# Optimization experiments

Measured on AMD Instinct MI355X. Metric: run time of the kernel, lower is better.

The kernel has to match this reference:

```python
import jax, jax.numpy as jnp
import numpy as np

TOPK = 2
ALPHA = 32.0
EPS = 1e-20


def setup_inputs() -> dict:
    key = jax.random.key(0)
    ks = jax.random.split(key, 6)
    E, D, R, Q, V = 16, 2048, 16, 2048, 512
    B, S = 2, 2048
    return {
        "hidden_states": jax.random.normal(ks[0], (B, S, D), jnp.float32),
        "router_weight": jax.random.normal(ks[1], (E, D), jnp.float32) * 0.02,
        "q_lora_a": jax.random.normal(ks[2], (E, D, R), jnp.float32) * 0.02,
        "q_lora_b": jax.random.normal(ks[3], (E, R, Q), jnp.float32) * 0.02,
        "v_lora_a": jax.random.normal(ks[4], (E, D, R), jnp.float32) * 0.02,
        "v_lora_b": jax.random.normal(ks[5], (E, R, V), jnp.float32) * 0.02,
    }


def reference(hidden_states, router_weight, q_lora_a, q_lora_b, v_lora_a, v_lora_b):
    E, D, R = q_lora_a.shape
    Qo = q_lora_b.shape[-1]
    Vo = v_lora_b.shape[-1]
    scale = ALPHA / float(R)
    orig_shape = hidden_states.shape[:-1]
    h = hidden_states.reshape(-1, D)  # [n, D]
    n = h.shape[0]

    # router: top-k softmax probs, renormalized over the k selected experts
    logits = jnp.einsum('nd,ed->ne', h, router_weight)
    probs = jax.nn.softmax(logits, axis=-1)
    scores, idx = jax.lax.top_k(probs, TOPK)          # [n, k]
    scores = scores / (scores.sum(-1, keepdims=True) + EPS)

    # per-token expert combine weights c[n, e] = scale * sum_k score_k * 1[idx_k == e]
    c = jnp.zeros((n, E), h.dtype).at[jnp.arange(n)[:, None], idx].add(scores * scale)

    # dense per-expert low-rank projections; weighting by c makes non-selected
    # experts contribute zero -> identical math to gather + einsum + weighted sum.
    q_low = jnp.einsum('nd,edr->ner', h, q_lora_a) * c[..., None]  # [n, E, R]
    v_low = jnp.einsum('nd,edr->ner', h, v_lora_a) * c[..., None]
    q_delta = jnp.einsum('ner,erq->nq', q_low, q_lora_b)
    v_delta = jnp.einsum('ner,erv->nv', v_low, v_lora_b)

    return (q_delta.reshape(*orig_shape, Qo), v_delta.reshape(*orig_shape, Vo))
```

## Files before the change

kernel.cpp:

```cpp
#include <hip/hip_runtime.h>
#include <math.h>

#define DD 2048
#define EE 16
#define RR 16
#define QO 2048
#define VO 512
#define DSPLIT 4
#define DRANGE (DD / DSPLIT)
#define DC 64
#define ASTR 20
#define RDC 256
#define DSPL 8
#define TW 4
#define TBI (TW * 4)
#define ABLK 16
#define T2 32
#define CGQ (QO / 256)
#define CGV (VO / 256)

struct Route { int i0, i1; float w0, w1; };

__global__ __launch_bounds__(256) void logits_kernel(
    const float* __restrict__ h, const float* __restrict__ rw,
    double* __restrict__ lgp, int* __restrict__ cnt, int n)
{
    __shared__ float hs[8 * RDC];

    if (blockIdx.x == 0 && blockIdx.y == 0 && threadIdx.x < EE)
        cnt[threadIdx.x] = 0;

    int t0 = blockIdx.x * 8;
    int ds = blockIdx.y;
    int d0 = ds * RDC;
    int e  = threadIdx.x >> 4;
    int l  = threadIdx.x & 15;

    for (int i = threadIdx.x; i < 8 * (RDC / 4); i += 256) {
        int t = i >> 6, dq = (i & 63) * 4;
        float4 v = make_float4(0.f, 0.f, 0.f, 0.f);
        if (t0 + t < n)
            v = *(const float4*)&h[(size_t)(t0 + t) * DD + d0 + dq];
        *(float4*)&hs[t * RDC + dq] = v;
    }
    __syncthreads();

    double acc[8];
#pragma unroll
    for (int t = 0; t < 8; ++t) acc[t] = 0.0;

    const float* rwe = rw + e * DD + d0;
#pragma unroll
    for (int g = 0; g < RDC / 64; ++g) {
        int d = g * 64 + l * 4;
        float4 r4 = *(const float4*)&rwe[d];
        double rx = r4.x, ry = r4.y, rz = r4.z, rw4 = r4.w;
#pragma unroll
        for (int t = 0; t < 8; ++t) {
            float4 hv = *(const float4*)&hs[t * RDC + d];
            acc[t] += (double)hv.x * rx + (double)hv.y * ry
                    + (double)hv.z * rz + (double)hv.w * rw4;
        }
    }
#pragma unroll
    for (int t = 0; t < 8; ++t) {
#pragma unroll
        for (int off = 8; off; off >>= 1)
            acc[t] += __shfl_down(acc[t], off, 16);
    }
    if (l == 0) {
#pragma unroll
        for (int t = 0; t < 8; ++t) {
            int tok = t0 + t;
            if (tok < n)
                lgp[((size_t)tok * DSPL + ds) * EE + e] = acc[t];
        }
    }
}

__global__ __launch_bounds__(256) void finalize_kernel(
    const double* __restrict__ lgp, Route* __restrict__ route,
    unsigned short* __restrict__ bucket, int* __restrict__ cnt, int n)
{
    int j   = threadIdx.x >> 4;
    int l   = threadIdx.x & 15;
    int tok = blockIdx.x * 16 + j;
    if (tok >= n) return;

    const double* p = lgp + (size_t)tok * (DSPL * EE) + l;
    double s = 0.0;
#pragma unroll
    for (int ds = 0; ds < DSPL; ++ds) s += p[ds * EE];

    double m1 = s; int i1 = l;
#pragma unroll
    for (int off = 8; off; off >>= 1) {
        double om = __shfl_xor(m1, off, 16);
        int    oi = __shfl_xor(i1, off, 16);
        if (om > m1 || (om == m1 && oi < i1)) { m1 = om; i1 = oi; }
    }
    double s2 = (l == i1) ? -1.0e300 : s;
    double m2 = s2; int i2 = l;
#pragma unroll
    for (int off = 8; off; off >>= 1) {
        double om = __shfl_xor(m2, off, 16);
        int    oi = __shfl_xor(i2, off, 16);
        if (om > m2 || (om == m2 && oi < i2)) { m2 = om; i2 = oi; }
    }
    if (l == 0) {
        double ed = exp(m2 - m1);
        double w0 = 2.0 / (1.0 + ed);
        Route rt;
        rt.i0 = i1; rt.i1 = i2;
        rt.w0 = (float)w0;
        rt.w1 = (float)(2.0 - w0);
        route[tok] = rt;
        int p0 = atomicAdd(&cnt[i1], 1);
        bucket[(size_t)i1 * n + p0] = (unsigned short)(tok * 2);
        int p1 = atomicAdd(&cnt[i2], 1);
        bucket[(size_t)i2 * n + p1] = (unsigned short)(tok * 2 + 1);
    }
}

__device__ __forceinline__ void loadh(float (&hv)[4][TW],
        const float* const (&hp)[TW], int d0) {
#pragma unroll
    for (int dd = 0; dd < 4; ++dd)
#pragma unroll
        for (int ti = 0; ti < TW; ++ti)
            hv[dd][ti] = hp[ti][d0 + dd * 16];
}

__device__ __forceinline__ void computeh(float (&accq)[TW][4], float (&accv)[TW][4],
        const float (&hv)[4][TW], const float* aq, const float* av,
        int d0, int s, int rp) {
#pragma unroll
    for (int dd = 0; dd < 4; ++dd) {
        int d = d0 + dd * 16 + s;
        float4 aqv = *(const float4*)&aq[d * ASTR + rp * 4];
        float4 avv = *(const float4*)&av[d * ASTR + rp * 4];
        const float* ap = &aqv.x;
        const float* vp = &avv.x;
#pragma unroll
        for (int ti = 0; ti < TW; ++ti) {
            float hvv = hv[dd][ti];
#pragma unroll
            for (int ri = 0; ri < 4; ++ri) {
                accq[ti][ri] = fmaf(hvv, ap[ri], accq[ti][ri]);
                accv[ti][ri] = fmaf(hvv, vp[ri], accv[ti][ri]);
            }
        }
    }
}

__global__ __launch_bounds__(256, 2) void a_kernel(
    const float* __restrict__ h, const Route* __restrict__ route,
    const unsigned short* __restrict__ bucket, const int* __restrict__ cnt,
    const float* __restrict__ qa, const float* __restrict__ va,
    float* __restrict__ low, int n)
{
    int e  = blockIdx.x;
    int ds = blockIdx.z;
    int cnt_e = cnt[e];
    if ((int)(blockIdx.y * TBI) >= cnt_e) return;

    __align__(16) __shared__ float aq_s[DRANGE * ASTR];
    __align__(16) __shared__ float av_s[DRANGE * ASTR];

    const int dbase = ds * DRANGE;
    const float* qa_e = qa + ((size_t)e * DD + dbase) * RR;
    const float* va_e = va + ((size_t)e * DD + dbase) * RR;

    for (int i = threadIdx.x; i < DRANGE * RR / 4; i += 256) {
        int d = i >> 2, rf = (i & 3) * 4;
        *(float4*)&aq_s[d * ASTR + rf] = *(const float4*)&qa_e[(size_t)i * 4];
        *(float4*)&av_s[d * ASTR + rf] = *(const float4*)&va_e[(size_t)i * 4];
    }
    __syncthreads();

    int lane = threadIdx.x & 63;
    int w    = threadIdx.x >> 6;
    int s    = lane & 15;
    int rp   = lane >> 4;

    for (int cb = blockIdx.y * TBI; cb < cnt_e; cb += gridDim.y * TBI) {
        int cw = cb + w * TW;
        if (cw >= cnt_e) continue;

        int sl = 0; float wt = 0.f;
        if (lane < TW && cw + lane < cnt_e) {
            sl = bucket[(size_t)e * n + cw + lane];
            Route rt = route[sl >> 1];
            wt = (sl & 1) ? rt.w1 : rt.w0;
        }
        const float* hp[TW];
        int   slots[TW];
        float wts[TW];
#pragma unroll
        for (int ti = 0; ti < TW; ++ti) {
            slots[ti] = __shfl(sl, ti);
            wts[ti]   = __shfl(wt, ti);
            hp[ti]    = h + (size_t)(slots[ti] >> 1) * DD + dbase + s;
        }

        float accq[TW][4], accv[TW][4];
#pragma unroll
        for (int ti = 0; ti < TW; ++ti)
#pragma unroll
            for (int ri = 0; ri < 4; ++ri) { accq[ti][ri] = 0.f; accv[ti][ri] = 0.f; }

        float hvA[4][TW], hvB[4][TW];
        loadh(hvA, hp, 0);
#pragma unroll
        for (int d0 = 0; d0 < DRANGE; d0 += 2 * DC) {
            loadh(hvB, hp, d0 + DC);
            computeh(accq, accv, hvA, aq_s, av_s, d0, s, rp);
            if (d0 + 2 * DC < DRANGE) loadh(hvA, hp, d0 + 2 * DC);
            computeh(accq, accv, hvB, aq_s, av_s, d0 + DC, s, rp);
        }

#pragma unroll
        for (int ti = 0; ti < TW; ++ti)
#pragma unroll
            for (int ri = 0; ri < 4; ++ri) {
#pragma unroll
                for (int off = 8; off; off >>= 1) {
                    accq[ti][ri] += __shfl_down(accq[ti][ri], off, 16);
                    accv[ti][ri] += __shfl_down(accv[ti][ri], off, 16);
                }
            }
        if (s == 0) {
#pragma unroll
            for (int ti = 0; ti < TW; ++ti) {
                if (cw + ti < cnt_e) {
                    int   sl2 = slots[ti];
                    float wt2 = wts[ti];
                    size_t base = ((size_t)sl2 * DSPLIT + ds) * 32;
                    float4 q4 = make_float4(accq[ti][0] * wt2, accq[ti][1] * wt2,
                                            accq[ti][2] * wt2, accq[ti][3] * wt2);
                    float4 v4 = make_float4(accv[ti][0] * wt2, accv[ti][1] * wt2,
                                            accv[ti][2] * wt2, accv[ti][3] * wt2);
                    *(float4*)&low[base + rp * 4]      = q4;
                    *(float4*)&low[base + 16 + rp * 4] = v4;
                }
            }
        }
    }
}

__global__ __launch_bounds__(256) void b_kernel(
    const Route* __restrict__ route, const float* __restrict__ low,
    const float* __restrict__ qb, const float* __restrict__ vb,
    float* __restrict__ outq, float* __restrict__ outv, int n)
{
    int t0 = blockIdx.x * T2;
    int cg = blockIdx.y;
    int tid = threadIdx.x;

    __shared__ float acc_s[T2 * 256];
    __shared__ float ls[T2 * 2 * RR];
    __shared__ int   elist[EE * T2];
    __shared__ int   ecnt[EE];
    __shared__ Route rts[T2];

    if (tid < EE) ecnt[tid] = 0;
    if (tid < T2) {
        int tok = t0 + tid;
        if (tok < n) rts[tid] = route[tok];
        else { rts[tid].i0 = -1; rts[tid].i1 = -1; rts[tid].w0 = 0.f; rts[tid].w1 = 0.f; }
    }
    __syncthreads();
    if (tid < T2 * 2) {
        int j = tid >> 1, k = tid & 1;
        int e = k ? rts[j].i1 : rts[j].i0;
        if (e >= 0) {
            int p = atomicAdd(&ecnt[e], 1);
            elist[e * T2 + p] = j * 2 + k;
        }
    }
    int side = (cg >= CGQ) ? 1 : 0;
    {
        int slot = tid >> 2, r4 = (tid & 3) * 4;
        int j = slot >> 1, k = slot & 1;
        int tok = t0 + j;
        float4 v = make_float4(0.f, 0.f, 0.f, 0.f);
        if (tok < n) {
            const float* lp = low + (size_t)(tok * 2 + k) * (DSPLIT * 32) + side * 16 + r4;
            float4 p0 = *(const float4*)(lp);
            float4 p1 = *(const float4*)(lp + 32);
            float4 p2 = *(const float4*)(lp + 64);
            float4 p3 = *(const float4*)(lp + 96);
            v.x = p0.x + p1.x + p2.x + p3.x;
            v.y = p0.y + p1.y + p2.y + p3.y;
            v.z = p0.z + p1.z + p2.z + p3.z;
            v.w = p0.w + p1.w + p2.w + p3.w;
        }
        *(float4*)&ls[slot * RR + r4] = v;
    }
#pragma unroll
    for (int j = 0; j < T2; ++j) acc_s[j * 256 + tid] = 0.f;
    __syncthreads();

    const float* bp; float* outp; int W, colbase;
    if (cg < CGQ) { bp = qb; outp = outq; W = QO; colbase = cg * 256; }
    else          { bp = vb; outp = outv; W = VO; colbase = (cg - CGQ) * 256; }
    int col = colbase + tid;

    float bcA[RR], bcB[RR];
    {
        const float* be = bp + col;
#pragma unroll
        for (int r = 0; r < RR; ++r) bcA[r] = be[(size_t)r * W];
    }

#define PROC_E(EI, BC)                                                      \
    {                                                                       \
        int c = ecnt[EI];                                                   \
        for (int ii = 0; ii < c; ++ii) {                                    \
            int sk = elist[(EI) * T2 + ii];                                 \
            const float* lp = &ls[sk * RR];                                 \
            float4 l0 = *(const float4*)(lp);                               \
            float4 l1 = *(const float4*)(lp + 4);                           \
            float4 l2 = *(const float4*)(lp + 8);                           \
            float4 l3 = *(const float4*)(lp + 12);                          \
            float v = 0.f;                                                  \
            v = fmaf(l0.x, BC[0],  v); v = fmaf(l0.y, BC[1],  v);           \
            v = fmaf(l0.z, BC[2],  v); v = fmaf(l0.w, BC[3],  v);           \
            v = fmaf(l1.x, BC[4],  v); v = fmaf(l1.y, BC[5],  v);           \
            v = fmaf(l1.z, BC[6],  v); v = fmaf(l1.w, BC[7],  v);           \
            v = fmaf(l2.x, BC[8],  v); v = fmaf(l2.y, BC[9],  v);           \
            v = fmaf(l2.z, BC[10], v); v = fmaf(l2.w, BC[11], v);           \
            v = fmaf(l3.x, BC[12], v); v = fmaf(l3.y, BC[13], v);           \
            v = fmaf(l3.z, BC[14], v); v = fmaf(l3.w, BC[15], v);           \
            acc_s[(sk >> 1) * 256 + tid] += v;   \
        }                                                                   \
    }

    for (int e = 0; e < EE; e += 2) {
        {
            const float* bn = bp + (size_t)(e + 1) * RR * W + col;
#pragma unroll
            for (int r = 0; r < RR; ++r) bcB[r] = bn[(size_t)r * W];
        }
        PROC_E(e, bcA);
        if (e + 2 < EE) {
            const float* bn = bp + (size_t)(e + 2) * RR * W + col;
#pragma unroll
            for (int r = 0; r < RR; ++r) bcA[r] = bn[(size_t)r * W];
        }
        PROC_E(e + 1, bcB);
    }
#undef PROC_E

#pragma unroll
    for (int j = 0; j < T2; ++j) {
        int tok = t0 + j;
        if (tok < n) outp[(size_t)tok * W + col] = acc_s[j * 256 + tid];
    }
}

extern "C" void kernel_launch(void* const* d_in, const int* in_sizes, int n_in,
                              void* d_out, int out_size, void* d_ws, size_t ws_size,
                              hipStream_t stream) {
    const float* h  = (const float*)d_in[0];
    const float* rw = (const float*)d_in[1];
    const float* qa = (const float*)d_in[2];
    const float* qb = (const float*)d_in[3];
    const float* va = (const float*)d_in[4];
    const float* vb = (const float*)d_in[5];

    int n = in_sizes[0] / DD;
    float* out  = (float*)d_out;
    float* outq = out;
    float* outv = out + (size_t)n * QO;

    char* ws = (char*)d_ws;
    Route* route = (Route*)ws;
    size_t off = ((size_t)n * sizeof(Route) + 255) & ~(size_t)255;
    int* cnt = (int*)(ws + off);
    off = (off + EE * sizeof(int) + 255) & ~(size_t)255;
    unsigned short* bucket = (unsigned short*)(ws + off);
    off = (off + (size_t)EE * n * sizeof(unsigned short) + 255) & ~(size_t)255;
    float* low = (float*)(ws + off);
    double* lgp = (double*)low;

    dim3 g1((n + 7) / 8, DSPL);
    logits_kernel<<<g1, 256, 0, stream>>>(h, rw, lgp, cnt, n);

    finalize_kernel<<<(n + 15) / 16, 256, 0, stream>>>(lgp, route, bucket, cnt, n);

    dim3 g2(EE, ABLK, DSPLIT);
    a_kernel<<<g2, 256, 0, stream>>>(h, route, bucket, cnt, qa, va, low, n);

    dim3 g3((n + T2 - 1) / T2, CGQ + CGV);
    b_kernel<<<g3, 256, 0, stream>>>(route, low, qb, vb, outq, outv, n);
}
```

Baseline: 214.3 us.

## Split D range eight ways, swizzle A-weight LDS layout, raise a_kernel occupancy

The a_kernel now splits the D dimension eight ways instead of four, which halves each block's shared-memory tile. The padded stride-20 LDS layout is replaced by a dense stride-16 layout with an XOR swizzle that avoids bank conflicts. Launch bounds move to 4 blocks per SM and ABLK is halved, so more blocks can be resident to hide latency. In exchange, each token carries twice as many partial low-rank sums, so the reduction loop in the second kernel reads more data and the A weights are loaded by more blocks.

```diff
diff --git a/kernel.cpp b/kernel.cpp
--- a/kernel.cpp
+++ b/kernel.cpp
@@ -6,20 +6,23 @@
 #define RR 16
 #define QO 2048
 #define VO 512
-#define DSPLIT 4
+#define DSPLIT 8
 #define DRANGE (DD / DSPLIT)
 #define DC 64
-#define ASTR 20
 #define RDC 256
 #define DSPL 8
 #define TW 4
 #define TBI (TW * 4)
-#define ABLK 16
+#define ABLK 8
 #define T2 32
 #define CGQ (QO / 256)
 #define CGV (VO / 256)
 
 struct Route { int i0, i1; float w0, w1; };
+
+__device__ __forceinline__ int apos(int d, int rq) {
+    return d * 16 + ((rq ^ ((d >> 1) & 3)) << 2);
+}
 
 __global__ __launch_bounds__(256) void logits_kernel(
     const float* __restrict__ h, const float* __restrict__ rw,
@@ -137,8 +140,8 @@
 #pragma unroll
     for (int dd = 0; dd < 4; ++dd) {
         int d = d0 + dd * 16 + s;
-        float4 aqv = *(const float4*)&aq[d * ASTR + rp * 4];
-        float4 avv = *(const float4*)&av[d * ASTR + rp * 4];
+        float4 aqv = *(const float4*)&aq[apos(d, rp)];
+        float4 avv = *(const float4*)&av[apos(d, rp)];
         const float* ap = &aqv.x;
         const float* vp = &avv.x;
 #pragma unroll
@@ -153,7 +156,7 @@
     }
 }
 
-__global__ __launch_bounds__(256, 2) void a_kernel(
+__global__ __launch_bounds__(256, 4) void a_kernel(
     const float* __restrict__ h, const Route* __restrict__ route,
     const unsigned short* __restrict__ bucket, const int* __restrict__ cnt,
     const float* __restrict__ qa, const float* __restrict__ va,
@@ -164,17 +167,18 @@
     int cnt_e = cnt[e];
     if ((int)(blockIdx.y * TBI) >= cnt_e) return;
 
-    __align__(16) __shared__ float aq_s[DRANGE * ASTR];
-    __align__(16) __shared__ float av_s[DRANGE * ASTR];
+    __align__(16) __shared__ float aq_s[DRANGE * RR];
+    __align__(16) __shared__ float av_s[DRANGE * RR];
 
     const int dbase = ds * DRANGE;
     const float* qa_e = qa + ((size_t)e * DD + dbase) * RR;
     const float* va_e = va + ((size_t)e * DD + dbase) * RR;
 
     for (int i = threadIdx.x; i < DRANGE * RR / 4; i += 256) {
-        int d = i >> 2, rf = (i & 3) * 4;
-        *(float4*)&aq_s[d * ASTR + rf] = *(const float4*)&qa_e[(size_t)i * 4];
-        *(float4*)&av_s[d * ASTR + rf] = *(const float4*)&va_e[(size_t)i * 4];
+        int d = i >> 2, rq = i & 3;
+        int dst = apos(d, rq);
+        *(float4*)&aq_s[dst] = *(const float4*)&qa_e[(size_t)i * 4];
+        *(float4*)&av_s[dst] = *(const float4*)&va_e[(size_t)i * 4];
     }
     __syncthreads();
 
@@ -286,14 +290,13 @@
         float4 v = make_float4(0.f, 0.f, 0.f, 0.f);
         if (tok < n) {
             const float* lp = low + (size_t)(tok * 2 + k) * (DSPLIT * 32) + side * 16 + r4;
-            float4 p0 = *(const float4*)(lp);
-            float4 p1 = *(const float4*)(lp + 32);
-            float4 p2 = *(const float4*)(lp + 64);
-            float4 p3 = *(const float4*)(lp + 96);
-            v.x = p0.x + p1.x + p2.x + p3.x;
-            v.y = p0.y + p1.y + p2.y + p3.y;
-            v.z = p0.z + p1.z + p2.z + p3.z;
-            v.w = p0.w + p1.w + p2.w + p3.w;
+            float4 acc4 = make_float4(0.f, 0.f, 0.f, 0.f);
+#pragma unroll
+            for (int dsp = 0; dsp < DSPLIT; ++dsp) {
+                float4 p = *(const float4*)(lp + dsp * 32);
+                acc4.x += p.x; acc4.y += p.y; acc4.z += p.z; acc4.w += p.w;
+            }
+            v = acc4;
         }
         *(float4*)&ls[slot * RR + r4] = v;
     }
```

Result: slower. 225.4 us (+5.1%).
